# Kernel optimization log

Hardware: AMD Instinct MI355X
Metric: run time of the kernel (lower is better)

Reference implementation:

```python
import jax, jax.numpy as jnp
import numpy as np

B, N_E, E_DIM = 131072, 1024, 64
BETA = 0.25


def setup_inputs() -> dict:
    key = jax.random.key(0)
    kz, kw = jax.random.split(key)
    z = jax.random.normal(kz, (B, E_DIM), dtype=jnp.float32)
    # nn.Embedding init: uniform(-1/n_e, 1/n_e)
    emb_w = jax.random.uniform(kw, (N_E, E_DIM), dtype=jnp.float32,
                               minval=-1.0 / N_E, maxval=1.0 / N_E)
    return {"z": z, "emb_w": emb_w}


def reference(z, emb_w):
    beta = jnp.float32(BETA)
    # pairwise squared distances: [B, n_e]
    d = (jnp.sum(z * z, axis=1, keepdims=True)
         + jnp.sum(emb_w * emb_w, axis=1)
         - 2.0 * jnp.einsum('bd,nd->bn', z, emb_w))
    idx = jnp.argmin(d, axis=1)                      # [B]
    z_q = jnp.take(emb_w, idx, axis=0)               # [B, e_dim]
    # legacy=False branch
    loss = (beta * jnp.mean((jax.lax.stop_gradient(z_q) - z) ** 2)
            + jnp.mean((z_q - jax.lax.stop_gradient(z)) ** 2))
    # straight-through estimator
    z_q_st = z + jax.lax.stop_gradient(z_q - z)
    # torch.var is unbiased (ddof=1)
    v = jnp.var(idx.astype(jnp.float32), ddof=1)
    return (z_q_st, loss, idx, v)
```

## Files before the change

kernel.cpp:

```cpp
#include <hip/hip_runtime.h>
#include <stdint.h>


typedef __attribute__((ext_vector_type(8))) __bf16 bf16x8;
typedef __attribute__((ext_vector_type(4))) float f32x4;

#define NBLK 2048
#define NTHR 256
#define OUT_LOSS 8388608
#define OUT_IDX  8388609
#define OUT_VAR  8519681

#define WS_LOSS 0
#define WS_S1   8192
#define WS_S2   16384
#define WS_EFRAG 24576
#define WS_EE   (24576 + 131072)

__global__ void vq_prep(const float* __restrict__ emb, char* __restrict__ ws) {
  bf16x8* efrag = (bf16x8*)(ws + WS_EFRAG);
  float* eeoff = (float*)(ws + WS_EE);
  const int t = blockIdx.x;
  const int l = threadIdx.x;
  const int n = t * 16 + (l & 15);
  const int kb0 = (l >> 4) * 8;
  const float* er = emb + n * 64;
  for (int j = 0; j < 2; ++j) {
    const int kb = j * 32 + kb0;
    bf16x8 h;
#pragma unroll
    for (int i = 0; i < 8; ++i) h[i] = (__bf16)(-2.0f * er[kb + i]);
    efrag[(t * 2 + j) * 64 + l] = h;
  }
  if (l < 16) {
    const float* e2 = emb + (t * 16 + l) * 64;
    float s = 0.f;
#pragma unroll
    for (int d = 0; d < 64; ++d) s += e2[d] * e2[d];
    eeoff[t * 16 + l] = s + 0.5f;
  }
}

__global__ void __launch_bounds__(NTHR, 4) vq_main(
    const float* __restrict__ z, const float* __restrict__ emb,
    float* __restrict__ out, char* __restrict__ ws) {
  const int tid = threadIdx.x;
  const int wave = tid >> 6, lane = tid & 63;
  const int lr = lane & 15, ksl = lane >> 4;
  const int k0 = ksl * 8;
  const int row_base = blockIdx.x * 64;

  bf16x8 zf[4][2];
  float zz[4];
#pragma unroll
  for (int r = 0; r < 4; ++r) {
    const float* zr = z + (size_t)(row_base + r * 16 + lr) * 64;
    float s = 0.f;
#pragma unroll
    for (int j = 0; j < 2; ++j) {
      f32x4 v0 = *(const f32x4*)(zr + j * 32 + k0);
      f32x4 v1 = *(const f32x4*)(zr + j * 32 + k0 + 4);
      bf16x8 h;
#pragma unroll
      for (int i = 0; i < 4; ++i) {
        h[i] = (__bf16)v0[i]; h[4 + i] = (__bf16)v1[i];
        s += v0[i] * v0[i] + v1[i] * v1[i];
      }
      zf[r][j] = h;
    }
    zz[r] = s;
  }

  unsigned mkey[4];
#pragma unroll
  for (int r = 0; r < 4; ++r) mkey[r] = 0xFFFFFFFFu;

  const bf16x8* efrag = (const bf16x8*)(ws + WS_EFRAG);
  const f32x4* eeoff = (const f32x4*)(ws + WS_EE);
#pragma unroll 2
  for (int tt = 0; tt < 16; ++tt) {
    const int t = wave * 16 + tt;
    bf16x8 e0 = efrag[(t * 2 + 0) * 64 + lane];
    bf16x8 e1 = efrag[(t * 2 + 1) * 64 + lane];
    f32x4 ee = eeoff[t * 4 + ksl];
    const unsigned nb = (unsigned)(t * 16 + ksl * 4);
#pragma unroll
    for (int r = 0; r < 4; ++r) {
      f32x4 acc = __builtin_amdgcn_mfma_f32_16x16x32_bf16(e0, zf[r][0], ee, 0, 0, 0);
      acc = __builtin_amdgcn_mfma_f32_16x16x32_bf16(e1, zf[r][1], acc, 0, 0, 0);
#pragma unroll
      for (int j = 0; j < 4; ++j) {
        unsigned key = (__float_as_uint(acc[j]) & 0xFFFFFC00u) | (nb + j);
        mkey[r] = min(mkey[r], key);
      }
    }
  }

#pragma unroll
  for (int r = 0; r < 4; ++r) {
    mkey[r] = min(mkey[r], (unsigned)__shfl_xor((int)mkey[r], 16, 64));
    mkey[r] = min(mkey[r], (unsigned)__shfl_xor((int)mkey[r], 32, 64));
    zz[r] += __shfl_xor(zz[r], 16, 64);
    zz[r] += __shfl_xor(zz[r], 32, 64);
  }

  __shared__ unsigned skey[4][64];
  __shared__ float szz[64];
  __shared__ float sL[4];
  __shared__ int sA[4], sB[4];
  if (ksl == 0) {
#pragma unroll
    for (int r = 0; r < 4; ++r) {
      skey[wave][r * 16 + lr] = mkey[r];
      if (wave == 0) szz[r * 16 + lr] = zz[r];
    }
  }
  __syncthreads();

  const int row = tid >> 2, seg = tid & 3;
  const unsigned k = min(min(skey[0][row], skey[1][row]),
                         min(skey[2][row], skey[3][row]));
  const unsigned idx = k & 1023u;
  const size_t rowg = (size_t)row_base + row;
  const f32x4* ep = (const f32x4*)(emb + (size_t)idx * 64 + seg * 16);
  f32x4* op = (f32x4*)(out + rowg * 64 + seg * 16);
#pragma unroll
  for (int c = 0; c < 4; ++c) op[c] = ep[c];

  float ls = 0.f; int s1 = 0, s2 = 0;
  if (seg == 0) {
    ls = szz[row] + __uint_as_float(k & 0xFFFFFC00u) - 0.5f;
    s1 = (int)idx;
    s2 = (int)(idx * idx);
    out[OUT_IDX + rowg] = (float)idx;
  }
#pragma unroll
  for (int off = 1; off < 64; off <<= 1) {
    ls += __shfl_xor(ls, off, 64);
    s1 += __shfl_xor(s1, off, 64);
    s2 += __shfl_xor(s2, off, 64);
  }
  if (lane == 0) { sL[wave] = ls; sA[wave] = s1; sB[wave] = s2; }
  __syncthreads();
  if (tid == 0) {
    float L = 0; int a = 0, b = 0;
#pragma unroll
    for (int w = 0; w < 4; ++w) { L += sL[w]; a += sA[w]; b += sB[w]; }
    ((float*)(ws + WS_LOSS))[blockIdx.x] = L;
    ((int*)(ws + WS_S1))[blockIdx.x] = a;
    ((int*)(ws + WS_S2))[blockIdx.x] = b;
  }
}

__global__ void vq_final(float* __restrict__ out, const char* __restrict__ ws) {
  const int t = threadIdx.x;
  const float* lp = (const float*)(ws + WS_LOSS);
  const int* p1 = (const int*)(ws + WS_S1);
  const int* p2 = (const int*)(ws + WS_S2);
  double L = 0; long long a = 0, b = 0;
#pragma unroll
  for (int kk = 0; kk < 8; ++kk) {
    const int i = t + 256 * kk;
    L += (double)lp[i];
    a += (long long)p1[i];
    b += (long long)p2[i];
  }
#pragma unroll
  for (int off = 1; off < 64; off <<= 1) {
    L += __shfl_xor(L, off, 64);
    a += __shfl_xor(a, off, 64);
    b += __shfl_xor(b, off, 64);
  }
  __shared__ double sL[4];
  __shared__ long long sA[4], sB[4];
  const int wave = t >> 6, lane = t & 63;
  if (lane == 0) { sL[wave] = L; sA[wave] = a; sB[wave] = b; }
  __syncthreads();
  if (t == 0) {
    double Lt = 0; long long at = 0, bt = 0;
#pragma unroll
    for (int w = 0; w < 4; ++w) { Lt += sL[w]; at += sA[w]; bt += sB[w]; }
    out[OUT_LOSS] = (float)(1.25 * Lt / 8388608.0);
    long long num = bt * 131072LL - at * at;
    out[OUT_VAR] = (float)((double)num / (131072.0 * 131071.0));
  }
}

extern "C" void kernel_launch(void* const* d_in, const int* in_sizes, int n_in,
                              void* d_out, int out_size, void* d_ws, size_t ws_size,
                              hipStream_t stream) {
  (void)in_sizes; (void)n_in; (void)out_size; (void)ws_size;
  const float* z = (const float*)d_in[0];
  const float* emb = (const float*)d_in[1];
  float* out = (float*)d_out;
  char* ws = (char*)d_ws;
  vq_prep<<<64, 64, 0, stream>>>(emb, ws);
  vq_main<<<NBLK, NTHR, 0, stream>>>(z, emb, out, ws);
  vq_final<<<1, 256, 0, stream>>>(out, ws);
}
```

Measured before the change: 55.45 us.

## Software-pipeline codebook fragment loads and interleave MFMA with key reduction

Fully unrolls the codebook loop into 8 steps of two tiles each, with a double-buffered prefetch of the next pair of codebook fragments and offsets issued between the MFMA groups. All MFMAs for a step are issued before the min-key reduction, so global load latency and MFMA latency can overlap the VALU work. The row squared-norm reduction moves to wave 0 only, which frees registers. The launch-bounds occupancy hint is dropped, so the compiler may use more registers at the cost of possibly lower occupancy.

Result: faster. 50.55 us (-8.8%).

```diff
diff --git a/kernel.cpp b/kernel.cpp
--- a/kernel.cpp
+++ b/kernel.cpp
@@ -41,7 +41,7 @@
   }
 }
 
-__global__ void __launch_bounds__(NTHR, 4) vq_main(
+__global__ void __launch_bounds__(NTHR) vq_main(
     const float* __restrict__ z, const float* __restrict__ emb,
     float* __restrict__ out, char* __restrict__ ws) {
   const int tid = threadIdx.x;
@@ -50,70 +50,100 @@
   const int k0 = ksl * 8;
   const int row_base = blockIdx.x * 64;
 
-  bf16x8 zf[4][2];
-  float zz[4];
-#pragma unroll
-  for (int r = 0; r < 4; ++r) {
-    const float* zr = z + (size_t)(row_base + r * 16 + lr) * 64;
-    float s = 0.f;
-#pragma unroll
-    for (int j = 0; j < 2; ++j) {
-      f32x4 v0 = *(const f32x4*)(zr + j * 32 + k0);
-      f32x4 v1 = *(const f32x4*)(zr + j * 32 + k0 + 4);
-      bf16x8 h;
-#pragma unroll
-      for (int i = 0; i < 4; ++i) {
-        h[i] = (__bf16)v0[i]; h[4 + i] = (__bf16)v1[i];
-        s += v0[i] * v0[i] + v1[i] * v1[i];
-      }
-      zf[r][j] = h;
-    }
-    zz[r] = s;
-  }
-
-  unsigned mkey[4];
-#pragma unroll
-  for (int r = 0; r < 4; ++r) mkey[r] = 0xFFFFFFFFu;
-
-  const bf16x8* efrag = (const bf16x8*)(ws + WS_EFRAG);
-  const f32x4* eeoff = (const f32x4*)(ws + WS_EE);
-#pragma unroll 2
-  for (int tt = 0; tt < 16; ++tt) {
-    const int t = wave * 16 + tt;
-    bf16x8 e0 = efrag[(t * 2 + 0) * 64 + lane];
-    bf16x8 e1 = efrag[(t * 2 + 1) * 64 + lane];
-    f32x4 ee = eeoff[t * 4 + ksl];
-    const unsigned nb = (unsigned)(t * 16 + ksl * 4);
-#pragma unroll
-    for (int r = 0; r < 4; ++r) {
-      f32x4 acc = __builtin_amdgcn_mfma_f32_16x16x32_bf16(e0, zf[r][0], ee, 0, 0, 0);
-      acc = __builtin_amdgcn_mfma_f32_16x16x32_bf16(e1, zf[r][1], acc, 0, 0, 0);
-#pragma unroll
-      for (int j = 0; j < 4; ++j) {
-        unsigned key = (__float_as_uint(acc[j]) & 0xFFFFFC00u) | (nb + j);
-        mkey[r] = min(mkey[r], key);
-      }
-    }
-  }
-
-#pragma unroll
-  for (int r = 0; r < 4; ++r) {
-    mkey[r] = min(mkey[r], (unsigned)__shfl_xor((int)mkey[r], 16, 64));
-    mkey[r] = min(mkey[r], (unsigned)__shfl_xor((int)mkey[r], 32, 64));
-    zz[r] += __shfl_xor(zz[r], 16, 64);
-    zz[r] += __shfl_xor(zz[r], 32, 64);
-  }
-
   __shared__ unsigned skey[4][64];
   __shared__ float szz[64];
   __shared__ float sL[4];
   __shared__ int sA[4], sB[4];
+
+  bf16x8 zf[4][2];
+  {
+#pragma unroll
+    for (int r = 0; r < 4; ++r) {
+      const float* zr = z + (size_t)(row_base + r * 16 + lr) * 64;
+      float s = 0.f;
+#pragma unroll
+      for (int j = 0; j < 2; ++j) {
+        f32x4 v0 = *(const f32x4*)(zr + j * 32 + k0);
+        f32x4 v1 = *(const f32x4*)(zr + j * 32 + k0 + 4);
+        bf16x8 h;
+#pragma unroll
+        for (int i = 0; i < 4; ++i) {
+          h[i] = (__bf16)v0[i]; h[4 + i] = (__bf16)v1[i];
+          s += v0[i] * v0[i] + v1[i] * v1[i];
+        }
+        zf[r][j] = h;
+      }
+      if (wave == 0) {
+        s += __shfl_xor(s, 16, 64);
+        s += __shfl_xor(s, 32, 64);
+        if (ksl == 0) szz[r * 16 + lr] = s;
+      }
+    }
+  }
+
+  unsigned mkey[4];
+#pragma unroll
+  for (int r = 0; r < 4; ++r) mkey[r] = 0xFFFFFFFFu;
+
+  const bf16x8* efrag = (const bf16x8*)(ws + WS_EFRAG);
+  const f32x4* eeoff = (const f32x4*)(ws + WS_EE);
+  const int tbase = wave * 16;
+
+  bf16x8 e0b[2][2], e1b[2][2];
+  f32x4 eeb[2][2];
+#pragma unroll
+  for (int s = 0; s < 2; ++s) {
+    const int t = tbase + s;
+    e0b[0][s] = efrag[(t * 2 + 0) * 64 + lane];
+    e1b[0][s] = efrag[(t * 2 + 1) * 64 + lane];
+    eeb[0][s] = eeoff[t * 4 + ksl];
+  }
+
+#pragma unroll
+  for (int p = 0; p < 8; ++p) {
+    const int cur = p & 1, nxt = cur ^ 1;
+    f32x4 acc[2][4];
+#pragma unroll
+    for (int r = 0; r < 4; ++r) {
+      f32x4 a = __builtin_amdgcn_mfma_f32_16x16x32_bf16(e0b[cur][0], zf[r][0], eeb[cur][0], 0, 0, 0);
+      acc[0][r] = __builtin_amdgcn_mfma_f32_16x16x32_bf16(e1b[cur][0], zf[r][1], a, 0, 0, 0);
+    }
+    if (p < 7) {
+#pragma unroll
+      for (int s = 0; s < 2; ++s) {
+        const int t = tbase + (p + 1) * 2 + s;
+        e0b[nxt][s] = efrag[(t * 2 + 0) * 64 + lane];
+        e1b[nxt][s] = efrag[(t * 2 + 1) * 64 + lane];
+        eeb[nxt][s] = eeoff[t * 4 + ksl];
+      }
+    }
+#pragma unroll
+    for (int r = 0; r < 4; ++r) {
+      f32x4 a = __builtin_amdgcn_mfma_f32_16x16x32_bf16(e0b[cur][1], zf[r][0], eeb[cur][1], 0, 0, 0);
+      acc[1][r] = __builtin_amdgcn_mfma_f32_16x16x32_bf16(e1b[cur][1], zf[r][1], a, 0, 0, 0);
+    }
+#pragma unroll
+    for (int s = 0; s < 2; ++s) {
+      const unsigned nb = (unsigned)((tbase + p * 2 + s) * 16 + ksl * 4);
+#pragma unroll
+      for (int r = 0; r < 4; ++r) {
+#pragma unroll
+        for (int j = 0; j < 4; ++j) {
+          const unsigned key = (__float_as_uint(acc[s][r][j]) & 0xFFFFFC00u) | (nb + j);
+          mkey[r] = min(mkey[r], key);
+        }
+      }
+    }
+  }
+
+#pragma unroll
+  for (int r = 0; r < 4; ++r) {
+    mkey[r] = min(mkey[r], (unsigned)__shfl_xor((int)mkey[r], 16, 64));
+    mkey[r] = min(mkey[r], (unsigned)__shfl_xor((int)mkey[r], 32, 64));
+  }
   if (ksl == 0) {
 #pragma unroll
-    for (int r = 0; r < 4; ++r) {
-      skey[wave][r * 16 + lr] = mkey[r];
-      if (wave == 0) szz[r * 16 + lr] = zz[r];
-    }
+    for (int r = 0; r < 4; ++r) skey[wave][r * 16 + lr] = mkey[r];
   }
   __syncthreads();
 
```

## Split VQ main kernel into distance/argmin and gather/reduce kernels

Applied to the files above, without the earlier changes.

Splits the fused kernel into a distance kernel and an output kernel. The distance kernel uses 1024-thread blocks, with each of 16 waves holding 64 codebook entries in registers. Each block processes 128 rows, combining per-wave minima through shared-memory atomicMin and writing keys and row norms to the workspace. A second kernel gathers codebook rows and does the loss and variance partial sums. This removes the per-wave codebook loop and its reloads, but costs an extra launch and a workspace round trip, and every z row is now loaded by 16 waves instead of 4.

Result: slower. 211.5 us (+281.4%).

```diff
diff --git a/kernel.cpp b/kernel.cpp
--- a/kernel.cpp
+++ b/kernel.cpp
@@ -5,17 +5,17 @@
 typedef __attribute__((ext_vector_type(8))) __bf16 bf16x8;
 typedef __attribute__((ext_vector_type(4))) float f32x4;
 
-#define NBLK 2048
-#define NTHR 256
 #define OUT_LOSS 8388608
 #define OUT_IDX  8388609
 #define OUT_VAR  8519681
 
-#define WS_LOSS 0
-#define WS_S1   8192
-#define WS_S2   16384
+#define WS_LOSS  0
+#define WS_S1    8192
+#define WS_S2    16384
 #define WS_EFRAG 24576
-#define WS_EE   (24576 + 131072)
+#define WS_EE    (24576 + 131072)
+#define WS_KEY   (WS_EE + 4096)
+#define WS_ZZ    (WS_KEY + 524288)
 
 __global__ void vq_prep(const float* __restrict__ emb, char* __restrict__ ws) {
   bf16x8* efrag = (bf16x8*)(ws + WS_EFRAG);
@@ -41,85 +41,111 @@
   }
 }
 
-__global__ void __launch_bounds__(NTHR, 4) vq_main(
-    const float* __restrict__ z, const float* __restrict__ emb,
-    float* __restrict__ out, char* __restrict__ ws) {
+__global__ void __launch_bounds__(1024, 4) vq_dist(
+    const float* __restrict__ z, char* __restrict__ ws) {
   const int tid = threadIdx.x;
   const int wave = tid >> 6, lane = tid & 63;
   const int lr = lane & 15, ksl = lane >> 4;
   const int k0 = ksl * 8;
-  const int row_base = blockIdx.x * 64;
-
-  bf16x8 zf[4][2];
-  float zz[4];
-#pragma unroll
-  for (int r = 0; r < 4; ++r) {
-    const float* zr = z + (size_t)(row_base + r * 16 + lr) * 64;
-    float s = 0.f;
-#pragma unroll
-    for (int j = 0; j < 2; ++j) {
-      f32x4 v0 = *(const f32x4*)(zr + j * 32 + k0);
-      f32x4 v1 = *(const f32x4*)(zr + j * 32 + k0 + 4);
-      bf16x8 h;
-#pragma unroll
-      for (int i = 0; i < 4; ++i) {
-        h[i] = (__bf16)v0[i]; h[4 + i] = (__bf16)v1[i];
-        s += v0[i] * v0[i] + v1[i] * v1[i];
-      }
-      zf[r][j] = h;
-    }
-    zz[r] = s;
-  }
-
-  unsigned mkey[4];
-#pragma unroll
-  for (int r = 0; r < 4; ++r) mkey[r] = 0xFFFFFFFFu;
+
+  __shared__ unsigned skey[64];
+  __shared__ float szz[64];
 
   const bf16x8* efrag = (const bf16x8*)(ws + WS_EFRAG);
   const f32x4* eeoff = (const f32x4*)(ws + WS_EE);
-#pragma unroll 2
-  for (int tt = 0; tt < 16; ++tt) {
-    const int t = wave * 16 + tt;
-    bf16x8 e0 = efrag[(t * 2 + 0) * 64 + lane];
-    bf16x8 e1 = efrag[(t * 2 + 1) * 64 + lane];
-    f32x4 ee = eeoff[t * 4 + ksl];
-    const unsigned nb = (unsigned)(t * 16 + ksl * 4);
+  bf16x8 e0b[4], e1b[4];
+  f32x4 eeb[4];
+#pragma unroll
+  for (int tt = 0; tt < 4; ++tt) {
+    const int t = wave * 4 + tt;
+    e0b[tt] = efrag[(t * 2 + 0) * 64 + lane];
+    e1b[tt] = efrag[(t * 2 + 1) * 64 + lane];
+    eeb[tt] = eeoff[t * 4 + ksl];
+  }
+
+  unsigned* wskey = (unsigned*)(ws + WS_KEY);
+  float* wszz = (float*)(ws + WS_ZZ);
+
+  for (int s = 0; s < 2; ++s) {
+    const int row_base = (blockIdx.x * 2 + s) * 64;
+    if (tid < 64) skey[tid] = 0xFFFFFFFFu;
+    __syncthreads();
+
+    bf16x8 zf[4][2];
+    float zz[4];
 #pragma unroll
     for (int r = 0; r < 4; ++r) {
-      f32x4 acc = __builtin_amdgcn_mfma_f32_16x16x32_bf16(e0, zf[r][0], ee, 0, 0, 0);
-      acc = __builtin_amdgcn_mfma_f32_16x16x32_bf16(e1, zf[r][1], acc, 0, 0, 0);
-#pragma unroll
-      for (int j = 0; j < 4; ++j) {
-        unsigned key = (__float_as_uint(acc[j]) & 0xFFFFFC00u) | (nb + j);
-        mkey[r] = min(mkey[r], key);
+      const float* zr = z + (size_t)(row_base + r * 16 + lr) * 64;
+      float acc = 0.f;
+#pragma unroll
+      for (int j = 0; j < 2; ++j) {
+        f32x4 v0 = *(const f32x4*)(zr + j * 32 + k0);
+        f32x4 v1 = *(const f32x4*)(zr + j * 32 + k0 + 4);
+        bf16x8 h;
+#pragma unroll
+        for (int i = 0; i < 4; ++i) {
+          h[i] = (__bf16)v0[i]; h[4 + i] = (__bf16)v1[i];
+          if (wave == 0) acc += v0[i] * v0[i] + v1[i] * v1[i];
+        }
+        zf[r][j] = h;
       }
-    }
-  }
-
-#pragma unroll
-  for (int r = 0; r < 4; ++r) {
-    mkey[r] = min(mkey[r], (unsigned)__shfl_xor((int)mkey[r], 16, 64));
-    mkey[r] = min(mkey[r], (unsigned)__shfl_xor((int)mkey[r], 32, 64));
-    zz[r] += __shfl_xor(zz[r], 16, 64);
-    zz[r] += __shfl_xor(zz[r], 32, 64);
-  }
-
-  __shared__ unsigned skey[4][64];
-  __shared__ float szz[64];
-  __shared__ float sL[4];
-  __shared__ int sA[4], sB[4];
-  if (ksl == 0) {
+      zz[r] = acc;
+    }
+
+    unsigned mkey[4];
+#pragma unroll
+    for (int r = 0; r < 4; ++r) mkey[r] = 0xFFFFFFFFu;
+
+#pragma unroll
+    for (int tt = 0; tt < 4; ++tt) {
+      const unsigned nb = (unsigned)((wave * 4 + tt) * 16 + ksl * 4);
+#pragma unroll
+      for (int r = 0; r < 4; ++r) {
+        f32x4 a = __builtin_amdgcn_mfma_f32_16x16x32_bf16(e0b[tt], zf[r][0], eeb[tt], 0, 0, 0);
+        a = __builtin_amdgcn_mfma_f32_16x16x32_bf16(e1b[tt], zf[r][1], a, 0, 0, 0);
+        const unsigned key0 = (__float_as_uint(a[0]) & 0xFFFFFC00u) | (nb + 0);
+        const unsigned key1 = (__float_as_uint(a[1]) & 0xFFFFFC00u) | (nb + 1);
+        const unsigned key2 = (__float_as_uint(a[2]) & 0xFFFFFC00u) | (nb + 2);
+        const unsigned key3 = (__float_as_uint(a[3]) & 0xFFFFFC00u) | (nb + 3);
+        mkey[r] = min(min(min(key0, key1), key2), min(key3, mkey[r]));
+      }
+    }
+
 #pragma unroll
     for (int r = 0; r < 4; ++r) {
-      skey[wave][r * 16 + lr] = mkey[r];
-      if (wave == 0) szz[r * 16 + lr] = zz[r];
-    }
-  }
-  __syncthreads();
-
+      mkey[r] = min(mkey[r], (unsigned)__shfl_xor((int)mkey[r], 16, 64));
+      mkey[r] = min(mkey[r], (unsigned)__shfl_xor((int)mkey[r], 32, 64));
+      if (ksl == 0) atomicMin(&skey[r * 16 + lr], mkey[r]);
+    }
+    if (wave == 0) {
+#pragma unroll
+      for (int r = 0; r < 4; ++r) {
+        zz[r] += __shfl_xor(zz[r], 16, 64);
+        zz[r] += __shfl_xor(zz[r], 32, 64);
+        if (ksl == 0) szz[r * 16 + lr] = zz[r];
+      }
+    }
+    __syncthreads();
+    if (tid < 64) {
+      wskey[row_base + tid] = skey[tid];
+      wszz[row_base + tid] = szz[tid];
+    }
+    __syncthreads();
+  }
+}
+
+__global__ void __launch_bounds__(256) vq_out(
+    const float* __restrict__ emb, float* __restrict__ out,
+    char* __restrict__ ws) {
+  const int tid = threadIdx.x;
+  const int wave = tid >> 6, lane = tid & 63;
+  const int row_base = blockIdx.x * 64;
   const int row = tid >> 2, seg = tid & 3;
-  const unsigned k = min(min(skey[0][row], skey[1][row]),
-                         min(skey[2][row], skey[3][row]));
+
+  const unsigned* wskey = (const unsigned*)(ws + WS_KEY);
+  const float* wszz = (const float*)(ws + WS_ZZ);
+
+  const unsigned k = wskey[row_base + row];
   const unsigned idx = k & 1023u;
   const size_t rowg = (size_t)row_base + row;
   const f32x4* ep = (const f32x4*)(emb + (size_t)idx * 64 + seg * 16);
@@ -129,7 +155,7 @@
 
   float ls = 0.f; int s1 = 0, s2 = 0;
   if (seg == 0) {
-    ls = szz[row] + __uint_as_float(k & 0xFFFFFC00u) - 0.5f;
+    ls = wszz[row_base + row] + __uint_as_float(k & 0xFFFFFC00u) - 0.5f;
     s1 = (int)idx;
     s2 = (int)(idx * idx);
     out[OUT_IDX + rowg] = (float)idx;
@@ -140,6 +166,8 @@
     s1 += __shfl_xor(s1, off, 64);
     s2 += __shfl_xor(s2, off, 64);
   }
+  __shared__ float sL[4];
+  __shared__ int sA[4], sB[4];
   if (lane == 0) { sL[wave] = ls; sA[wave] = s1; sB[wave] = s2; }
   __syncthreads();
   if (tid == 0) {
@@ -195,6 +223,7 @@
   float* out = (float*)d_out;
   char* ws = (char*)d_ws;
   vq_prep<<<64, 64, 0, stream>>>(emb, ws);
-  vq_main<<<NBLK, NTHR, 0, stream>>>(z, emb, out, ws);
+  vq_dist<<<1024, 1024, 0, stream>>>(z, ws);
+  vq_out<<<2048, 256, 0, stream>>>(emb, out, ws);
   vq_final<<<1, 256, 0, stream>>>(out, ws);
 }
```
